# Performance work log

Measured on AMD Instinct MI355X. Metric: run time of the kernel, lower is better.

## Reference

```python
import jax, jax.numpy as jnp
import numpy as np

H, L, N = 1024, 2048, 32
EPS = 1e-7


def _hippo_lambda(n):
    # make_NPLR_HiPPO(2n) -> eigenvalues of skew part, keep first n with imag>0, shift by -0.5
    i = np.arange(2 * n, dtype=np.float64)
    x = 2 * i + 1
    hippo = np.tril(np.sqrt(np.outer(x, x)), k=-1)
    skew = (hippo - hippo.T) / 2
    lam = np.linalg.eig(skew)[0]
    idx = np.nonzero(lam.imag > 0)[0][:n]
    lam_sel = lam[idx] - 0.5
    return np.stack([lam_sel.real, lam_sel.imag], -1).astype(np.float32)


def setup_inputs() -> dict:
    key = jax.random.key(0)
    k1, k2, k3 = jax.random.split(key, 3)
    u = jax.random.normal(k1, (H, L), dtype=jnp.float32)
    # lecun-style scale for W (fan_in ~ N)
    W = jax.random.normal(k2, (H, N, 2), dtype=jnp.float32) / np.float32(np.sqrt(N))
    # log_step_initializer(dt_min=1e-3, dt_max=0.1)
    log_step = jax.random.uniform(k3, (H,), dtype=jnp.float32) * np.float32(np.log(0.1) - np.log(1e-3)) + np.float32(np.log(1e-3))
    Lambda_ri = jnp.asarray(_hippo_lambda(N))
    D = jnp.ones((H,), dtype=jnp.float32)
    return {"u": u, "W": W, "Lambda_ri": Lambda_ri, "log_step": log_step, "D": D}


def _complex_softmax(x):
    # softmax over complex vector, stabilized by the entry with max real part
    x2 = x - x[jnp.argmax(x.real)]
    e = jnp.exp(x2)
    s = jnp.sum(e)
    return e * (s.conj() / (s * s.conj() + EPS))


def _dss_kernel(Wc, Lam, step, length):
    # P: (N, L) complex; kernel = (W / Lambda) @ complex_softmax_rows(P)
    P = (step * Lam)[:, None] * jnp.arange(length)
    S = jax.vmap(_complex_softmax)(P)
    return ((Wc / Lam) @ S).real  # (L,)


def _fft_conv(u, K):
    # non-circular convolution via zero-padded rfft of length 2L
    n = u.shape[0]
    ud = jnp.fft.rfft(jnp.pad(u, (0, n)))
    Kd = jnp.fft.rfft(jnp.pad(K, (0, n)))
    return jnp.fft.irfft(ud * Kd)[:n]


def reference(u, W, Lambda_ri, log_step, D):
    Lam = Lambda_ri[:, 0] + 1j * Lambda_ri[:, 1]  # shared HiPPO eigenvalues (N,)
    Wc = W[..., 0] + 1j * W[..., 1]               # (H, N) complex
    step = jnp.exp(log_step)                      # (H,)

    def per_channel(u_h, W_h, step_h, D_h):
        K = _dss_kernel(W_h, Lam, step_h, u_h.shape[0])
        return _fft_conv(u_h, K) + D_h * u_h

    return jax.vmap(per_channel)(u, Wc, step, D)
```

## Files before the change

### kernel.cpp

```cpp
#include <hip/hip_runtime.h>
#include <math.h>


static constexpr int kH = 1024;
static constexpr int kL = 2048;
static constexpr int kN = 32;
static constexpr int kChunk = 32;
static constexpr int kMpW = 16;
static constexpr float kEps = 1e-7f;

__global__ void dss_setup_kernel(const float* __restrict__ W,
                                 const float* __restrict__ Lambda_ri,
                                 const float* __restrict__ log_step,
                                 float* __restrict__ zc) {
    int idx = blockIdx.x * blockDim.x + threadIdx.x;
    if (idx >= kH * kN) return;
    int h = idx / kN;
    int n = idx % kN;

    float step = expf(log_step[h]);
    float lr = Lambda_ri[2 * n + 0];
    float li = Lambda_ri[2 * n + 1];
    float wr = W[(h * kN + n) * 2 + 0];
    float wi = W[(h * kN + n) * 2 + 1];

    float ar = step * lr;
    float ai = step * li;

    float ea = expf(ar);
    float sb, cb;
    sincosf(ai, &sb, &cb);
    float zr = ea * cb, zi = ea * sb;

    float em = expm1f(ar);
    float sh = sinf(0.5f * ai);
    float dr = fmaf(-em, cb, 2.f * sh * sh);
    float di = -ea * sb;

    float eL = expf(ar * (float)kL);
    float sL, cL;
    sincosf(ai * (float)kL, &sL, &cL);
    float nr = 1.f - eL * cL;
    float ni = -eL * sL;

    float dd = dr * dr + di * di;
    float id = 1.f / dd;
    float sr = (nr * dr + ni * di) * id;
    float si = (ni * dr - nr * di) * id;

    float ll = lr * lr + li * li;
    float il = 1.f / ll;
    float qr = (wr * lr + wi * li) * il;
    float qi = (wi * lr - wr * li) * il;

    float ss = fmaf(sr, sr, fmaf(si, si, kEps));
    float is = 1.f / ss;
    float cr = (qr * sr + qi * si) * is;
    float ci = (qi * sr - qr * si) * is;

    float eC = expf(ar * (float)kChunk);
    float sC, cC;
    sincosf(ai * (float)kChunk, &sC, &cC);

    float* o = zc + idx * 8;
    o[0] = zr;      o[1] = zi;
    o[2] = cr;      o[3] = ci;
    o[4] = eC * cC; o[5] = eC * sC;
    o[6] = 0.f;     o[7] = 0.f;
}

__global__ __launch_bounds__(128, 2)
void dss_scan_kernel(const float* __restrict__ u,
                     const float* __restrict__ zc,
                     const float* __restrict__ Dv,
                     float* __restrict__ y) {
    __shared__ float u_s[kL + (kL >> 5)];
    __shared__ float y0_s[kL + (kL >> 5)];
    __shared__ float y1_s[kL + (kL >> 5)];

    const int h = blockIdx.x;
    const int tid = threadIdx.x;
    const int wave = tid >> 6;
    const int lane = tid & 63;

    const float* uh = u + (size_t)h * kL;
    for (int i = tid; i < kL; i += 128) u_s[i + (i >> 5)] = uh[i];

    const float* zch = zc + ((size_t)h * kN + wave * kMpW) * 8;
    float zr[kMpW], zi[kMpW], cr[kMpW], ci[kMpW];
#pragma unroll
    for (int n = 0; n < kMpW; ++n) {
        zr[n] = zch[n * 8 + 0];
        zi[n] = zch[n * 8 + 1];
        cr[n] = zch[n * 8 + 2];
        ci[n] = zch[n * 8 + 3];
    }
    __syncthreads();

    float er[kMpW], ei[kMpW];
#pragma unroll
    for (int n = 0; n < kMpW; ++n) { er[n] = 0.f; ei[n] = 0.f; }

    const int base = lane * kChunk;
    for (int k = 0; k < kChunk; ++k) {
        const int i = base + k;
        const float uv = u_s[i + (i >> 5)];
#pragma unroll
        for (int n = 0; n < kMpW; ++n) {
            const float tr = zi[n] * er[n];
            er[n] = fmaf(zr[n], er[n], fmaf(-zi[n], ei[n], uv));
            ei[n] = fmaf(zr[n], ei[n], tr);
        }
    }

#pragma unroll
    for (int n = 0; n < kMpW; ++n) {
        float vr = __shfl_up(er[n], 1);
        float vi = __shfl_up(ei[n], 1);
        er[n] = (lane >= 1) ? vr : 0.f;
        ei[n] = (lane >= 1) ? vi : 0.f;
    }
    float pr[kMpW], pi[kMpW];
#pragma unroll
    for (int n = 0; n < kMpW; ++n) { pr[n] = zch[n * 8 + 4]; pi[n] = zch[n * 8 + 5]; }

#pragma unroll
    for (int d = 1; d < 64; d <<= 1) {
#pragma unroll
        for (int n = 0; n < kMpW; ++n) {
            float vr = __shfl_up(er[n], d);
            float vi = __shfl_up(ei[n], d);
            const bool ok = (lane >= d);
            vr = ok ? vr : 0.f;
            vi = ok ? vi : 0.f;
            er[n] = fmaf(pr[n], vr, fmaf(-pi[n], vi, er[n]));
            ei[n] = fmaf(pr[n], vi, fmaf(pi[n], vr, ei[n]));
        }
        if (d < 32) {
#pragma unroll
            for (int n = 0; n < kMpW; ++n) {
                const float t = fmaf(pr[n], pr[n], -pi[n] * pi[n]);
                pi[n] = 2.f * pr[n] * pi[n];
                pr[n] = t;
            }
        }
    }

    const float Dh = Dv[h];
    float* ys = wave ? y1_s : y0_s;
    for (int k = 0; k < kChunk; ++k) {
        const int i = base + k;
        const float uv = u_s[i + (i >> 5)];
        float acc = wave ? 0.f : Dh * uv;
#pragma unroll
        for (int n = 0; n < kMpW; ++n) {
            const float tr = zi[n] * er[n];
            er[n] = fmaf(zr[n], er[n], fmaf(-zi[n], ei[n], uv));
            ei[n] = fmaf(zr[n], ei[n], tr);
            acc = fmaf(cr[n], er[n], acc);
            acc = fmaf(-ci[n], ei[n], acc);
        }
        ys[i + (i >> 5)] = acc;
    }
    __syncthreads();

    float* yh = y + (size_t)h * kL;
    for (int i = tid; i < kL; i += 128) {
        yh[i] = y0_s[i + (i >> 5)] + y1_s[i + (i >> 5)];
    }
}

extern "C" void kernel_launch(void* const* d_in, const int* in_sizes, int n_in,
                              void* d_out, int out_size, void* d_ws, size_t ws_size,
                              hipStream_t stream) {
    const float* u        = (const float*)d_in[0];
    const float* W        = (const float*)d_in[1];
    const float* Lam      = (const float*)d_in[2];
    const float* log_step = (const float*)d_in[3];
    const float* Dv       = (const float*)d_in[4];
    float* y  = (float*)d_out;
    float* zc = (float*)d_ws;

    dss_setup_kernel<<<(kH * kN + 255) / 256, 256, 0, stream>>>(W, Lam, log_step, zc);
    dss_scan_kernel<<<kH, 128, 0, stream>>>(u, zc, Dv, y);
}
```

Measured before the change: 89.72 us.

## Fuse setup into scan kernel and split modes across four waves

Moves the per-channel parameter setup (exp, sincos, complex divides) into the scan kernel, with 32 threads writing coefficients to shared memory, which removes the second launch and the workspace round trip. Blocks grow to four waves of 256 threads, each owning 8 modes instead of 16, which lowers register pressure and raises parallelism per channel. Per-wave outputs are combined through shared-memory atomicAdd rather than separate buffers, and the D*u skip term moves to the final store. The costs are atomic contention on LDS and a serial setup phase at the start of every block.

```diff
diff --git a/kernel.cpp b/kernel.cpp
--- a/kernel.cpp
+++ b/kernel.cpp
@@ -6,77 +6,20 @@
 static constexpr int kL = 2048;
 static constexpr int kN = 32;
 static constexpr int kChunk = 32;
-static constexpr int kMpW = 16;
+static constexpr int kWaves = 4;
+static constexpr int kMpW = kN / kWaves;
 static constexpr float kEps = 1e-7f;
 
-__global__ void dss_setup_kernel(const float* __restrict__ W,
-                                 const float* __restrict__ Lambda_ri,
-                                 const float* __restrict__ log_step,
-                                 float* __restrict__ zc) {
-    int idx = blockIdx.x * blockDim.x + threadIdx.x;
-    if (idx >= kH * kN) return;
-    int h = idx / kN;
-    int n = idx % kN;
-
-    float step = expf(log_step[h]);
-    float lr = Lambda_ri[2 * n + 0];
-    float li = Lambda_ri[2 * n + 1];
-    float wr = W[(h * kN + n) * 2 + 0];
-    float wi = W[(h * kN + n) * 2 + 1];
-
-    float ar = step * lr;
-    float ai = step * li;
-
-    float ea = expf(ar);
-    float sb, cb;
-    sincosf(ai, &sb, &cb);
-    float zr = ea * cb, zi = ea * sb;
-
-    float em = expm1f(ar);
-    float sh = sinf(0.5f * ai);
-    float dr = fmaf(-em, cb, 2.f * sh * sh);
-    float di = -ea * sb;
-
-    float eL = expf(ar * (float)kL);
-    float sL, cL;
-    sincosf(ai * (float)kL, &sL, &cL);
-    float nr = 1.f - eL * cL;
-    float ni = -eL * sL;
-
-    float dd = dr * dr + di * di;
-    float id = 1.f / dd;
-    float sr = (nr * dr + ni * di) * id;
-    float si = (ni * dr - nr * di) * id;
-
-    float ll = lr * lr + li * li;
-    float il = 1.f / ll;
-    float qr = (wr * lr + wi * li) * il;
-    float qi = (wi * lr - wr * li) * il;
-
-    float ss = fmaf(sr, sr, fmaf(si, si, kEps));
-    float is = 1.f / ss;
-    float cr = (qr * sr + qi * si) * is;
-    float ci = (qi * sr - qr * si) * is;
-
-    float eC = expf(ar * (float)kChunk);
-    float sC, cC;
-    sincosf(ai * (float)kChunk, &sC, &cC);
-
-    float* o = zc + idx * 8;
-    o[0] = zr;      o[1] = zi;
-    o[2] = cr;      o[3] = ci;
-    o[4] = eC * cC; o[5] = eC * sC;
-    o[6] = 0.f;     o[7] = 0.f;
-}
-
-__global__ __launch_bounds__(128, 2)
-void dss_scan_kernel(const float* __restrict__ u,
-                     const float* __restrict__ zc,
-                     const float* __restrict__ Dv,
-                     float* __restrict__ y) {
+__global__ __launch_bounds__(256, 4)
+void dss_fused_kernel(const float* __restrict__ u,
+                      const float* __restrict__ W,
+                      const float* __restrict__ Lambda_ri,
+                      const float* __restrict__ log_step,
+                      const float* __restrict__ Dv,
+                      float* __restrict__ y) {
     __shared__ float u_s[kL + (kL >> 5)];
-    __shared__ float y0_s[kL + (kL >> 5)];
-    __shared__ float y1_s[kL + (kL >> 5)];
+    __shared__ float y_s[kL + (kL >> 5)];
+    __shared__ float p_s[kN][6];
 
     const int h = blockIdx.x;
     const int tid = threadIdx.x;
@@ -84,18 +27,72 @@
     const int lane = tid & 63;
 
     const float* uh = u + (size_t)h * kL;
-    for (int i = tid; i < kL; i += 128) u_s[i + (i >> 5)] = uh[i];
+    for (int i = tid; i < kL; i += 256) {
+        u_s[i + (i >> 5)] = uh[i];
+        y_s[i + (i >> 5)] = 0.f;
+    }
 
-    const float* zch = zc + ((size_t)h * kN + wave * kMpW) * 8;
+    if (tid < kN) {
+        const int n = tid;
+        const float step = expf(log_step[h]);
+        const float lr = Lambda_ri[2 * n + 0];
+        const float li = Lambda_ri[2 * n + 1];
+        const float wr = W[(h * kN + n) * 2 + 0];
+        const float wi = W[(h * kN + n) * 2 + 1];
+
+        const float ar = step * lr;
+        const float ai = step * li;
+
+        const float ea = expf(ar);
+        float sb, cb;
+        sincosf(ai, &sb, &cb);
+
+        const float em = expm1f(ar);
+        const float sh = sinf(0.5f * ai);
+        const float dr = fmaf(-em, cb, 2.f * sh * sh);
+        const float di = -ea * sb;
+
+        const float eL = expf(ar * (float)kL);
+        float sL, cL;
+        sincosf(ai * (float)kL, &sL, &cL);
+        const float nr = 1.f - eL * cL;
+        const float ni = -eL * sL;
+
+        const float dd = dr * dr + di * di;
+        const float id = 1.f / dd;
+        const float sr = (nr * dr + ni * di) * id;
+        const float si = (ni * dr - nr * di) * id;
+
+        const float ll = lr * lr + li * li;
+        const float il = 1.f / ll;
+        const float qr = (wr * lr + wi * li) * il;
+        const float qi = (wi * lr - wr * li) * il;
+
+        const float ss = fmaf(sr, sr, fmaf(si, si, kEps));
+        const float is = 1.f / ss;
+
+        const float eC = expf(ar * (float)kChunk);
+        float sC, cC;
+        sincosf(ai * (float)kChunk, &sC, &cC);
+
+        p_s[n][0] = ea * cb;
+        p_s[n][1] = ea * sb;
+        p_s[n][2] = (qr * sr + qi * si) * is;
+        p_s[n][3] = (qi * sr - qr * si) * is;
+        p_s[n][4] = eC * cC;
+        p_s[n][5] = eC * sC;
+    }
+    __syncthreads();
+
+    const int m0 = wave * kMpW;
     float zr[kMpW], zi[kMpW], cr[kMpW], ci[kMpW];
 #pragma unroll
     for (int n = 0; n < kMpW; ++n) {
-        zr[n] = zch[n * 8 + 0];
-        zi[n] = zch[n * 8 + 1];
-        cr[n] = zch[n * 8 + 2];
-        ci[n] = zch[n * 8 + 3];
+        zr[n] = p_s[m0 + n][0];
+        zi[n] = p_s[m0 + n][1];
+        cr[n] = p_s[m0 + n][2];
+        ci[n] = p_s[m0 + n][3];
     }
-    __syncthreads();
 
     float er[kMpW], ei[kMpW];
 #pragma unroll
@@ -115,15 +112,17 @@
 
 #pragma unroll
     for (int n = 0; n < kMpW; ++n) {
-        float vr = __shfl_up(er[n], 1);
-        float vi = __shfl_up(ei[n], 1);
+        const float vr = __shfl_up(er[n], 1);
+        const float vi = __shfl_up(ei[n], 1);
         er[n] = (lane >= 1) ? vr : 0.f;
         ei[n] = (lane >= 1) ? vi : 0.f;
     }
     float pr[kMpW], pi[kMpW];
 #pragma unroll
-    for (int n = 0; n < kMpW; ++n) { pr[n] = zch[n * 8 + 4]; pi[n] = zch[n * 8 + 5]; }
-
+    for (int n = 0; n < kMpW; ++n) {
+        pr[n] = p_s[m0 + n][4];
+        pi[n] = p_s[m0 + n][5];
+    }
 #pragma unroll
     for (int d = 1; d < 64; d <<= 1) {
 #pragma unroll
@@ -146,12 +145,10 @@
         }
     }
 
-    const float Dh = Dv[h];
-    float* ys = wave ? y1_s : y0_s;
     for (int k = 0; k < kChunk; ++k) {
         const int i = base + k;
         const float uv = u_s[i + (i >> 5)];
-        float acc = wave ? 0.f : Dh * uv;
+        float acc = 0.f;
 #pragma unroll
         for (int n = 0; n < kMpW; ++n) {
             const float tr = zi[n] * er[n];
@@ -160,13 +157,14 @@
             acc = fmaf(cr[n], er[n], acc);
             acc = fmaf(-ci[n], ei[n], acc);
         }
-        ys[i + (i >> 5)] = acc;
+        atomicAdd(&y_s[i + (i >> 5)], acc);
     }
     __syncthreads();
 
+    const float Dh = Dv[h];
     float* yh = y + (size_t)h * kL;
-    for (int i = tid; i < kL; i += 128) {
-        yh[i] = y0_s[i + (i >> 5)] + y1_s[i + (i >> 5)];
+    for (int i = tid; i < kL; i += 256) {
+        yh[i] = fmaf(Dh, u_s[i + (i >> 5)], y_s[i + (i >> 5)]);
     }
 }
 
@@ -178,9 +176,7 @@
     const float* Lam      = (const float*)d_in[2];
     const float* log_step = (const float*)d_in[3];
     const float* Dv       = (const float*)d_in[4];
-    float* y  = (float*)d_out;
-    float* zc = (float*)d_ws;
+    float* y = (float*)d_out;
 
-    dss_setup_kernel<<<(kH * kN + 255) / 256, 256, 0, stream>>>(W, Lam, log_step, zc);
-    dss_scan_kernel<<<kH, 128, 0, stream>>>(u, zc, Dv, y);
+    dss_fused_kernel<<<kH, 256, 0, stream>>>(u, W, Lam, log_step, Dv, y);
 }
```

Result: slower. 118.4 us (+32.0%).

## Split state modes over four waves and keep input chunk in registers

Applied to the files above, without the earlier changes.

The per-channel scan block goes from two waves of 16 modes each to four waves of 8 modes each, so there are twice as many threads per channel and each thread does half the recurrence work and carries fewer registers. Each lane now loads its 32 input samples straight from global memory with float4 reads into registers instead of staging u through shared memory, which also removes the first barrier. Per-wave partial outputs go to a four-row shared buffer and are summed at writeback. The cost is more redundant global reads of u, since every wave loads it, plus the larger shared buffer and the four-way reduction.

```diff
diff --git a/kernel.cpp b/kernel.cpp
--- a/kernel.cpp
+++ b/kernel.cpp
@@ -6,8 +6,10 @@
 static constexpr int kL = 2048;
 static constexpr int kN = 32;
 static constexpr int kChunk = 32;
-static constexpr int kMpW = 16;
+static constexpr int kWaves = 4;
+static constexpr int kMpW = kN / kWaves;
 static constexpr float kEps = 1e-7f;
+static constexpr int kYStride = kL + (kL >> 5) + 1;
 
 __global__ void dss_setup_kernel(const float* __restrict__ W,
                                  const float* __restrict__ Lambda_ri,
@@ -30,7 +32,6 @@
     float ea = expf(ar);
     float sb, cb;
     sincosf(ai, &sb, &cb);
-    float zr = ea * cb, zi = ea * sb;
 
     float em = expm1f(ar);
     float sh = sinf(0.5f * ai);
@@ -55,38 +56,42 @@
 
     float ss = fmaf(sr, sr, fmaf(si, si, kEps));
     float is = 1.f / ss;
-    float cr = (qr * sr + qi * si) * is;
-    float ci = (qi * sr - qr * si) * is;
 
     float eC = expf(ar * (float)kChunk);
     float sC, cC;
     sincosf(ai * (float)kChunk, &sC, &cC);
 
-    float* o = zc + idx * 8;
-    o[0] = zr;      o[1] = zi;
-    o[2] = cr;      o[3] = ci;
-    o[4] = eC * cC; o[5] = eC * sC;
-    o[6] = 0.f;     o[7] = 0.f;
+    float* o = zc + (size_t)idx * 8;
+    o[0] = ea * cb;              o[1] = ea * sb;
+    o[2] = (qr * sr + qi * si) * is;
+    o[3] = (qi * sr - qr * si) * is;
+    o[4] = eC * cC;              o[5] = eC * sC;
+    o[6] = 0.f;                  o[7] = 0.f;
 }
 
-__global__ __launch_bounds__(128, 2)
+__global__ __launch_bounds__(256, 4)
 void dss_scan_kernel(const float* __restrict__ u,
                      const float* __restrict__ zc,
                      const float* __restrict__ Dv,
                      float* __restrict__ y) {
-    __shared__ float u_s[kL + (kL >> 5)];
-    __shared__ float y0_s[kL + (kL >> 5)];
-    __shared__ float y1_s[kL + (kL >> 5)];
+    __shared__ float y_s[kWaves][kYStride];
 
     const int h = blockIdx.x;
     const int tid = threadIdx.x;
     const int wave = tid >> 6;
     const int lane = tid & 63;
 
-    const float* uh = u + (size_t)h * kL;
-    for (int i = tid; i < kL; i += 128) u_s[i + (i >> 5)] = uh[i];
+    const float4* uh4 = (const float4*)(u + (size_t)h * kL) + lane * 8;
+    float uu[kChunk];
+#pragma unroll
+    for (int k = 0; k < 8; ++k) {
+        const float4 v = uh4[k];
+        uu[4 * k + 0] = v.x; uu[4 * k + 1] = v.y;
+        uu[4 * k + 2] = v.z; uu[4 * k + 3] = v.w;
+    }
 
-    const float* zch = zc + ((size_t)h * kN + wave * kMpW) * 8;
+    const int m0 = __builtin_amdgcn_readfirstlane((tid >> 6) * kMpW);
+    const float* zch = zc + ((size_t)h * kN + m0) * 8;
     float zr[kMpW], zi[kMpW], cr[kMpW], ci[kMpW];
 #pragma unroll
     for (int n = 0; n < kMpW; ++n) {
@@ -95,16 +100,14 @@
         cr[n] = zch[n * 8 + 2];
         ci[n] = zch[n * 8 + 3];
     }
-    __syncthreads();
 
     float er[kMpW], ei[kMpW];
 #pragma unroll
     for (int n = 0; n < kMpW; ++n) { er[n] = 0.f; ei[n] = 0.f; }
 
-    const int base = lane * kChunk;
+#pragma unroll
     for (int k = 0; k < kChunk; ++k) {
-        const int i = base + k;
-        const float uv = u_s[i + (i >> 5)];
+        const float uv = uu[k];
 #pragma unroll
         for (int n = 0; n < kMpW; ++n) {
             const float tr = zi[n] * er[n];
@@ -115,15 +118,17 @@
 
 #pragma unroll
     for (int n = 0; n < kMpW; ++n) {
-        float vr = __shfl_up(er[n], 1);
-        float vi = __shfl_up(ei[n], 1);
+        const float vr = __shfl_up(er[n], 1);
+        const float vi = __shfl_up(ei[n], 1);
         er[n] = (lane >= 1) ? vr : 0.f;
         ei[n] = (lane >= 1) ? vi : 0.f;
     }
     float pr[kMpW], pi[kMpW];
 #pragma unroll
-    for (int n = 0; n < kMpW; ++n) { pr[n] = zch[n * 8 + 4]; pi[n] = zch[n * 8 + 5]; }
-
+    for (int n = 0; n < kMpW; ++n) {
+        pr[n] = zch[n * 8 + 4];
+        pi[n] = zch[n * 8 + 5];
+    }
 #pragma unroll
     for (int d = 1; d < 64; d <<= 1) {
 #pragma unroll
@@ -147,11 +152,11 @@
     }
 
     const float Dh = Dv[h];
-    float* ys = wave ? y1_s : y0_s;
+    float* ys = &y_s[wave][0] + lane * 33;
+#pragma unroll
     for (int k = 0; k < kChunk; ++k) {
-        const int i = base + k;
-        const float uv = u_s[i + (i >> 5)];
-        float acc = wave ? 0.f : Dh * uv;
+        const float uv = uu[k];
+        float acc = (wave == 0) ? Dh * uv : 0.f;
 #pragma unroll
         for (int n = 0; n < kMpW; ++n) {
             const float tr = zi[n] * er[n];
@@ -160,13 +165,14 @@
             acc = fmaf(cr[n], er[n], acc);
             acc = fmaf(-ci[n], ei[n], acc);
         }
-        ys[i + (i >> 5)] = acc;
+        ys[k] = acc;
     }
     __syncthreads();
 
     float* yh = y + (size_t)h * kL;
-    for (int i = tid; i < kL; i += 128) {
-        yh[i] = y0_s[i + (i >> 5)] + y1_s[i + (i >> 5)];
+    for (int i = tid; i < kL; i += 256) {
+        const int idx = i + (i >> 5);
+        yh[i] = (y_s[0][idx] + y_s[1][idx]) + (y_s[2][idx] + y_s[3][idx]);
     }
 }
 
@@ -182,5 +188,5 @@
     float* zc = (float*)d_ws;
 
     dss_setup_kernel<<<(kH * kN + 255) / 256, 256, 0, stream>>>(W, Lam, log_step, zc);
-    dss_scan_kernel<<<kH, 128, 0, stream>>>(u, zc, Dv, y);
+    dss_scan_kernel<<<kH, 256, 0, stream>>>(u, zc, Dv, y);
 }
```

New measurement: 90.62 us. No clear change (+1.0%).
